# Kernel optimization log

Measured on AMD Instinct MI355X. Metric: run time of the kernel, lower is better.

The kernel has to match this reference:

```python
import jax, jax.numpy as jnp
import numpy as np

RADIUS = float(1.5 * 6 * 0.025 / 2.0)  # filter_extent / 2 = 0.1125
N_FLUID, N_BOX, K_F, K_B = 16000, 8000, 64, 32
KS = 4  # kernel size per axis -> 64 bins
EPS = 1e-12


def _radius_neighbors(q, p, radius, K, exclude_self=False):
    Nq = q.shape[0]
    idx = np.zeros((Nq, K), np.int32)
    mask = np.zeros((Nq, K), bool)
    r2 = radius * radius
    kth = min(K, p.shape[0] - 1)
    for s in range(0, Nq, 2048):
        e = min(s + 2048, Nq)
        d2 = ((q[s:e, None, :] - p[None, :, :]) ** 2).sum(-1)
        if exclude_self:
            d2[np.arange(e - s), np.arange(s, e)] = np.inf
        part = np.argpartition(d2, kth, axis=1)[:, :K].astype(np.int32)
        dk = np.take_along_axis(d2, part, 1)
        m = dk <= r2
        part[~m] = 0
        idx[s:e] = part
        mask[s:e] = m
    return idx, mask


def ball_to_cube(d):
    """Volume-preserving map unit ball -> unit cube [-1,1]^3 (Open3D ball_to_cube_volume_preserving)."""
    x, y, z = d[..., 0], d[..., 1], d[..., 2]
    sq = x * x + y * y + z * z
    norm = jnp.sqrt(sq)
    # --- sphere -> cylinder (radius 1, height 2) ---
    xy_sq = x * x + y * y
    polar = (1.25 * z * z) > xy_sq
    s_pol = jnp.sqrt(3.0 * norm / (norm + jnp.abs(z) + EPS))
    s_eq = norm / jnp.sqrt(xy_sq + EPS)
    s = jnp.where(polar, s_pol, s_eq)
    xc = x * s
    yc = y * s
    zc = jnp.where(polar, jnp.sign(z) * norm, 1.5 * z)
    zero = sq < EPS
    xc = jnp.where(zero, 0.0, xc)
    yc = jnp.where(zero, 0.0, yc)
    zc = jnp.where(zero, 0.0, zc)
    # --- cylinder -> cube: inverse Shirley-Chiu concentric map on the xy disc ---
    rxy = jnp.sqrt(xc * xc + yc * yc)
    xbig = jnp.abs(xc) >= jnp.abs(yc)
    safe_x = jnp.where(jnp.abs(xc) > EPS, xc, 1.0)
    safe_y = jnp.where(jnp.abs(yc) > EPS, yc, 1.0)
    four_over_pi = 4.0 / np.pi
    u1 = jnp.sign(xc) * rxy
    v1 = u1 * four_over_pi * jnp.arctan(yc / safe_x)
    v2 = jnp.sign(yc) * rxy
    u2 = v2 * four_over_pi * jnp.arctan(xc / safe_y)
    u = jnp.where(xbig, u1, u2)
    v = jnp.where(xbig, v1, v2)
    zero_xy = rxy < EPS
    u = jnp.where(zero_xy, 0.0, u)
    v = jnp.where(zero_xy, 0.0, v)
    return jnp.stack([u, v, zc], axis=-1)


def cconv(feat_src, pos_src, pos_q, nbr_idx, nbr_mask, filt, bias):
    """ContinuousConv: trilinear (align_corners=True) filter interpolation, poly6 window, no normalization."""
    N = pos_q.shape[0]
    kz, ky, kx, cin, cout = filt.shape
    pj = pos_src[nbr_idx]                       # [N,K,3]
    fj = feat_src[nbr_idx]                      # [N,K,Cin]
    d = (pj - pos_q[:, None, :]) / RADIUS       # normalized offsets in unit ball
    r_sqr = jnp.sum(d * d, axis=-1)             # [N,K]
    win = jnp.clip((1.0 - r_sqr) ** 3, 0.0, 1.0) * nbr_mask.astype(fj.dtype)
    u = ball_to_cube(d)                         # [N,K,3] in [-1,1]
    ks = jnp.asarray([kx, ky, kz], d.dtype)
    g = (u * 0.5 + 0.5) * (ks - 1.0)            # align_corners=True grid coords
    i0 = jnp.clip(jnp.floor(g), 0.0, ks - 2.0).astype(jnp.int32)  # [N,K,3]
    t = g - i0                                  # trilinear fractions
    Fflat = filt.reshape(kz * ky * kx, cin, cout)
    A = jnp.zeros((N, kz * ky * kx, cin), fj.dtype)   # per-query bin accumulator
    n_idx = jnp.arange(N)[:, None]
    for dz in (0, 1):
        for dy in (0, 1):
            for dx in (0, 1):
                w = ((t[..., 0] if dx else 1.0 - t[..., 0])
                     * (t[..., 1] if dy else 1.0 - t[..., 1])
                     * (t[..., 2] if dz else 1.0 - t[..., 2])) * win
                bins = ((i0[..., 2] + dz) * ky + (i0[..., 1] + dy)) * kx + (i0[..., 0] + dx)
                A = A.at[n_idx, bins].add(w[..., None] * fj)
    return jnp.einsum('nbc,bco->no', A, Fflat) + bias


def _forward(pos, vel, box, box_feats,
             w_conv0_fluid, b_conv0_fluid, w_conv0_obstacle, b_conv0_obstacle,
             w_dense0, b_dense0, w_conv1, b_conv1, w_dense1, b_dense1,
             w_conv2, b_conv2, w_dense2, b_dense2,
             nbr_fluid_idx, nbr_fluid_mask, nbr_box_idx, nbr_box_mask):
    fluid_feats = jnp.concatenate([jnp.ones_like(pos[:, :1]), vel], axis=-1)  # [N,4]
    a_cf = cconv(fluid_feats, pos, pos, nbr_fluid_idx, nbr_fluid_mask, w_conv0_fluid, b_conv0_fluid)
    a_df = fluid_feats @ w_dense0 + b_dense0
    a_co = cconv(box_feats, box, pos, nbr_box_idx, nbr_box_mask, w_conv0_obstacle, b_conv0_obstacle)
    feats = jnp.concatenate([a_co, a_cf, a_df], axis=-1)                      # [N,96]
    inp1 = jax.nn.relu(feats)
    ans1 = cconv(inp1, pos, pos, nbr_fluid_idx, nbr_fluid_mask, w_conv1, b_conv1) + inp1 @ w_dense1 + b_dense1
    inp2 = jax.nn.relu(ans1)
    ans2 = (cconv(inp2, pos, pos, nbr_fluid_idx, nbr_fluid_mask, w_conv2, b_conv2)
            + inp2 @ w_dense2 + b_dense2 + ans1)                               # residual (64==64)
    return ans2  # particle_feat = ans_convs[-2] returned by forward()


def setup_inputs() -> dict:
    rng = np.random.default_rng(0)
    L = 1.357  # cube side chosen so avg neighbor count within RADIUS is ~48
    pos = rng.uniform(0, L, (N_FLUID, 3)).astype(np.float32)
    box = rng.uniform(0, L, (N_BOX, 3)).astype(np.float32)
    vel = (0.5 * rng.standard_normal((N_FLUID, 3))).astype(np.float32)
    nrm = rng.standard_normal((N_BOX, 3)).astype(np.float32)
    box_feats = nrm / np.linalg.norm(nrm, axis=-1, keepdims=True)
    nf_idx, nf_mask = _radius_neighbors(pos, pos, RADIUS, K_F, exclude_self=True)
    nb_idx, nb_mask = _radius_neighbors(pos, box, RADIUS, K_B, exclude_self=False)

    def filt(cin, cout):
        s = (6.0 / (cin * KS ** 3 + cout)) ** 0.5
        return (s * rng.standard_normal((KS, KS, KS, cin, cout))).astype(np.float32)

    def lin(cin, cout):
        s = (6.0 / (cin + cout)) ** 0.5
        return (s * rng.standard_normal((cin, cout))).astype(np.float32)

    z = lambda c: np.zeros((c,), np.float32)
    inp = dict(
        pos=pos, vel=vel, box=box, box_feats=box_feats,
        w_conv0_fluid=filt(4, 32), b_conv0_fluid=z(32),
        w_conv0_obstacle=filt(3, 32), b_conv0_obstacle=z(32),
        w_dense0=lin(4, 32), b_dense0=z(32),
        w_conv1=filt(96, 64), b_conv1=z(64), w_dense1=lin(96, 64), b_dense1=z(64),
        w_conv2=filt(64, 64), b_conv2=z(64), w_dense2=lin(64, 64), b_dense2=z(64),
        nbr_fluid_idx=nf_idx, nbr_fluid_mask=nf_mask,
        nbr_box_idx=nb_idx, nbr_box_mask=nb_mask,
    )
    return {k: jnp.asarray(v) for k, v in inp.items()}


def reference(pos, vel, box, box_feats,
              w_conv0_fluid, b_conv0_fluid, w_conv0_obstacle, b_conv0_obstacle,
              w_dense0, b_dense0, w_conv1, b_conv1, w_dense1, b_dense1,
              w_conv2, b_conv2, w_dense2, b_dense2,
              nbr_fluid_idx, nbr_fluid_mask, nbr_box_idx, nbr_box_mask):
    return _forward(pos, vel, box, box_feats,
                    w_conv0_fluid, b_conv0_fluid, w_conv0_obstacle, b_conv0_obstacle,
                    w_dense0, b_dense0, w_conv1, b_conv1, w_dense1, b_dense1,
                    w_conv2, b_conv2, w_dense2, b_dense2,
                    nbr_fluid_idx, nbr_fluid_mask, nbr_box_idx, nbr_box_mask)
```

## Files before the change

kernel.cpp:

```cpp
#include <hip/hip_runtime.h>
#include <cstdint>

#define DEVFN __device__ __forceinline__

using hh8 = __attribute__((ext_vector_type(8))) _Float16;
using f4  = __attribute__((ext_vector_type(4))) float;

constexpr float RAD  = 0.1125f;
constexpr float R2C  = RAD * RAD;
constexpr float EPSF = 1e-12f;
constexpr float FOPI = 1.27323954473516268615f;

DEVFN float sgnf(float a){ return (a > 0.f) ? 1.f : ((a < 0.f) ? -1.f : 0.f); }

DEVFN unsigned short f2h(float f){
  _Float16 h = (_Float16)f;
  union { _Float16 h; unsigned short u; } x; x.h = h; return x.u;
}
DEVFN hh8 ld_hh8(const unsigned short* p){ return *(const hh8*)p; }

DEVFN void nbr_geom(float ddx, float ddy, float ddz, float factor, int* bins, float* w8)
{
  float x = ddx / RAD, y = ddy / RAD, z = ddz / RAD;
  float sq = x*x + y*y + z*z;
  float omr = 1.f - sq;
  float win = (omr > 0.f) ? omr*omr*omr : 0.f;
  win *= factor;
  float nrm   = sqrtf(sq);
  float xy_sq = x*x + y*y;
  bool  polar = (1.25f*z*z) > xy_sq;
  float s = polar ? sqrtf(3.f*nrm/(nrm + fabsf(z) + EPSF))
                  : (nrm / sqrtf(xy_sq + EPSF));
  float xc = x*s, yc = y*s;
  float zc = polar ? (sgnf(z)*nrm) : (1.5f*z);
  if (sq < EPSF){ xc = 0.f; yc = 0.f; zc = 0.f; }
  float rxy  = sqrtf(xc*xc + yc*yc);
  bool  xbig = fabsf(xc) >= fabsf(yc);
  float sx = (fabsf(xc) > EPSF) ? xc : 1.f;
  float sy = (fabsf(yc) > EPSF) ? yc : 1.f;
  float u1 = sgnf(xc)*rxy;
  float v1 = u1 * FOPI * atanf(yc / sx);
  float v2 = sgnf(yc)*rxy;
  float u2 = v2 * FOPI * atanf(xc / sy);
  float u = xbig ? u1 : u2;
  float v = xbig ? v1 : v2;
  if (rxy < EPSF){ u = 0.f; v = 0.f; }
  float gx = (u *0.5f + 0.5f)*3.f;
  float gy = (v *0.5f + 0.5f)*3.f;
  float gz = (zc*0.5f + 0.5f)*3.f;
  float fx = fminf(fmaxf(floorf(gx), 0.f), 2.f);
  float fy = fminf(fmaxf(floorf(gy), 0.f), 2.f);
  float fz = fminf(fmaxf(floorf(gz), 0.f), 2.f);
  int ix = (int)fx, iy = (int)fy, iz = (int)fz;
  float tx = gx - fx, ty = gy - fy, tz = gz - fz;
  float wx[2] = {1.f - tx, tx};
  float wy[2] = {1.f - ty, ty};
  float wz[2] = {1.f - tz, tz};
  #pragma unroll
  for (int dz2 = 0; dz2 < 2; ++dz2)
    #pragma unroll
    for (int dy2 = 0; dy2 < 2; ++dy2)
      #pragma unroll
      for (int dx2 = 0; dx2 < 2; ++dx2){
        int c = (dz2 << 2) | (dy2 << 1) | dx2;
        bins[c] = ((iz + dz2)*4 + (iy + dy2))*4 + (ix + dx2);
        w8[c]   = wx[dx2]*wy[dy2]*wz[dz2]*win;
      }
}

__global__ __launch_bounds__(256)
void k_conv0(const float* __restrict__ pos, const float* __restrict__ vel,
             const float* __restrict__ box, const float* __restrict__ boxf,
             const float* __restrict__ Wfilt, const float* __restrict__ bcf,
             const float* __restrict__ Ofilt, const float* __restrict__ bco,
             const float* __restrict__ Wd0, const float* __restrict__ bd0,
             const int* __restrict__ nfi, const int* __restrict__ nbi,
             int KB, float* __restrict__ inp1)
{
  const int n = blockIdx.x, t = threadIdx.x;
  const int lane = t & 63, w = t >> 6, r = lane & 15, h = lane >> 4;

  __shared__ __align__(16) unsigned short LWf[64*64];
  __shared__ __align__(16) unsigned short LWo[64*32];
  __shared__ __align__(16) unsigned short LBf[16*64];
  __shared__ __align__(16) unsigned short LBo[16*32];
  __shared__ float Af[64*4];
  __shared__ float Ao[64*3];
  __shared__ int gjf[64]; __shared__ int gjo[32];
  __shared__ float red[256];

  const float qx = pos[3*n], qy = pos[3*n+1], qz = pos[3*n+2];
  int bins[8]; float w8[8];

  if (w == 0){
    const int k = lane;
    const int j = nfi[(size_t)n*64 + k];
    const float ddx = pos[3*j] - qx, ddy = pos[3*j+1] - qy, ddz = pos[3*j+2] - qz;
    const float d2 = ddx*ddx + ddy*ddy + ddz*ddz;
    unsigned long long zm = __ballot(j == 0);
    int fz = __ffsll(zm) - 1;
    float factor = (j != 0) ? 1.f : ((k == fz && d2 <= R2C && n != 0) ? 1.f : 0.f);
    nbr_geom(ddx, ddy, ddz, factor, bins, w8);
    gjf[k] = j;
  } else if (w == 1){
    const int k = lane;
    const bool act = k < KB;
    const int j = act ? nbi[(size_t)n*KB + k] : 1;
    float ddx = 0.f, ddy = 0.f, ddz = 0.f, d2 = 1e30f;
    if (act){
      ddx = box[3*j] - qx; ddy = box[3*j+1] - qy; ddz = box[3*j+2] - qz;
      d2 = ddx*ddx + ddy*ddy + ddz*ddz;
    }
    unsigned long long zm = __ballot(act && j == 0);
    int fz = __ffsll(zm) - 1;
    float factor = (j != 0) ? 1.f : ((k == fz && d2 <= R2C) ? 1.f : 0.f);
    nbr_geom(ddx, ddy, ddz, factor, bins, w8);
    if (act) gjo[k] = j;
  } else {
    int4 z4 = make_int4(0,0,0,0);
    for (int i = t-128; i < 512; i += 128) *(int4*)&LWf[i*8] = z4;
    for (int i = t-128; i < 256; i += 128) *(int4*)&LWo[i*8] = z4;
    if (t-128 < 128) *(int4*)&LBf[(t-128)*8] = z4;
    if (t-128 <  64) *(int4*)&LBo[(t-128)*8] = z4;
  }
  __syncthreads();

  if (w == 0){
    #pragma unroll
    for (int q = 0; q < 8; ++q){
      int b = bins[q];
      LWf[b*64 + (lane ^ ((b&7)<<3))] = f2h(w8[q]);
    }
  } else if (w == 1){
    if (lane < KB){
      #pragma unroll
      for (int q = 0; q < 8; ++q){
        int b = bins[q];
        LWo[b*32 + (lane ^ ((b&3)<<3))] = f2h(w8[q]);
      }
    }
  } else if (w == 2){
    const int k = lane; const int j = gjf[k];
    LBf[0*64 + k] = f2h(1.f);
    LBf[1*64 + (k ^ 8)]  = f2h(vel[3*j]);
    LBf[2*64 + (k ^ 16)] = f2h(vel[3*j+1]);
    LBf[3*64 + (k ^ 24)] = f2h(vel[3*j+2]);
  } else {
    if (lane < KB){
      const int k = lane; const int j = gjo[k];
      LBo[0*32 + k]        = f2h(boxf[3*j]);
      LBo[1*32 + (k ^ 8)]  = f2h(boxf[3*j+1]);
      LBo[2*32 + (k ^ 16)] = f2h(boxf[3*j+2]);
    }
  }
  __syncthreads();

  f4 aF = {0.f,0.f,0.f,0.f}, aO = {0.f,0.f,0.f,0.f};
  {
    const int b = 16*w + r;
    #pragma unroll
    for (int ks = 0; ks < 2; ++ks){
      hh8 a  = ld_hh8(&LWf[b*64 + (((ks*4+h) ^ (b&7))<<3)]);
      hh8 bb = ld_hh8(&LBf[r*64 + (((ks*4+h) ^ (r&7))<<3)]);
      aF = __builtin_amdgcn_mfma_f32_16x16x32_f16(a, bb, aF, 0,0,0);
    }
    hh8 a2 = ld_hh8(&LWo[b*32 + ((h ^ (b&3))<<3)]);
    hh8 b2 = ld_hh8(&LBo[r*32 + ((h ^ (r&3))<<3)]);
    aO = __builtin_amdgcn_mfma_f32_16x16x32_f16(a2, b2, aO, 0,0,0);
  }
  #pragma unroll
  for (int rr = 0; rr < 4; ++rr){
    int b2 = 16*w + h*4 + rr;
    if (r < 4) Af[b2*4 + r] = aF[rr];
    if (r < 3) Ao[b2*3 + r] = aO[rr];
  }
  __syncthreads();

  const int o = t & 31, g = t >> 5;
  float p1 = 0.f;
  for (int b2 = g*8; b2 < g*8 + 8; ++b2)
    #pragma unroll
    for (int c = 0; c < 4; ++c)
      p1 += Af[b2*4 + c] * Wfilt[(b2*4 + c)*32 + o];
  red[t] = p1;
  __syncthreads();
  float a_cf = 0.f;
  if (t < 32){ for (int g2 = 0; g2 < 8; ++g2) a_cf += red[t + 32*g2]; }
  __syncthreads();
  float p2 = 0.f;
  for (int b2 = g*8; b2 < g*8 + 8; ++b2)
    #pragma unroll
    for (int c = 0; c < 3; ++c)
      p2 += Ao[b2*3 + c] * Ofilt[(b2*3 + c)*32 + o];
  red[t] = p2;
  __syncthreads();
  if (t < 32){
    float a_co = 0.f;
    for (int g2 = 0; g2 < 8; ++g2) a_co += red[t + 32*g2];
    const float vx = vel[3*n], vy = vel[3*n+1], vz = vel[3*n+2];
    const float a_df = Wd0[t] + Wd0[32 + t]*vx + Wd0[64 + t]*vy + Wd0[96 + t]*vz;
    const size_t base = (size_t)n * 96;
    inp1[base +      t] = fmaxf(a_co + bco[t], 0.f);
    inp1[base + 32 + t] = fmaxf(a_cf + bcf[t], 0.f);
    inp1[base + 64 + t] = fmaxf(a_df + bd0[t], 0.f);
  }
}

template<int C>
__global__ __launch_bounds__(256)
void k1_scatter(const float* __restrict__ pos, const float* __restrict__ feat,
                const int* __restrict__ nfi, int n0, unsigned short* __restrict__ Abuf)
{
  constexpr int Kpad = 64*C + C + (C == 96 ? 32 : 0);
  constexpr int CT = C/16;
  const int nloc = blockIdx.x;
  const int n = n0 + nloc;
  const int t = threadIdx.x;
  const int lane = t & 63, w = t >> 6, r = lane & 15, h = lane >> 4;

  __shared__ __align__(16) unsigned short sh[4096 + C*64];
  unsigned short* W  = sh;
  unsigned short* BT = sh + 4096;
  __shared__ int gj[64];

  int bins[8]; float w8[8];
  if (w == 0){
    const float qx = pos[3*n], qy = pos[3*n+1], qz = pos[3*n+2];
    const int k = lane;
    const int j = nfi[(size_t)n*64 + k];
    const float ddx = pos[3*j] - qx, ddy = pos[3*j+1] - qy, ddz = pos[3*j+2] - qz;
    const float d2 = ddx*ddx + ddy*ddy + ddz*ddz;
    unsigned long long zm = __ballot(j == 0);
    int fz = __ffsll(zm) - 1;
    float factor = (j != 0) ? 1.f : ((k == fz && d2 <= R2C && n != 0) ? 1.f : 0.f);
    nbr_geom(ddx, ddy, ddz, factor, bins, w8);
    gj[k] = j;
  } else {
    int4 z4 = make_int4(0,0,0,0);
    for (int i = t - 64; i < 512; i += 192) *(int4*)&W[i*8] = z4;
  }
  __syncthreads();

  if (w == 0){
    #pragma unroll
    for (int q = 0; q < 8; ++q){
      int b = bins[q];
      W[b*64 + (lane ^ ((b&7)<<3))] = f2h(w8[q]);
    }
  }
  for (int i = t; i < C*64; i += 256){
    int k = i / C, c = i - k*C;
    int j = gj[k];
    BT[c*64 + (k ^ ((c&7)<<3))] = f2h(feat[(size_t)j*C + c]);
  }
  __syncthreads();

  f4 acc[CT];
  #pragma unroll
  for (int ct = 0; ct < CT; ++ct) acc[ct] = f4{0.f,0.f,0.f,0.f};
  const int b = 16*w + r;
  #pragma unroll
  for (int ks = 0; ks < 2; ++ks){
    hh8 a = ld_hh8(&W[b*64 + (((ks*4+h) ^ (b&7))<<3)]);
    #pragma unroll
    for (int ct = 0; ct < CT; ++ct){
      int c = ct*16 + r;
      hh8 bb = ld_hh8(&BT[c*64 + (((ks*4+h) ^ (c&7))<<3)]);
      acc[ct] = __builtin_amdgcn_mfma_f32_16x16x32_f16(a, bb, acc[ct], 0,0,0);
    }
  }
  __syncthreads();

  unsigned short* Aout = sh;
  #pragma unroll
  for (int ct = 0; ct < CT; ++ct){
    int c = ct*16 + r;
    #pragma unroll
    for (int rr = 0; rr < 4; ++rr){
      int b2 = 16*w + h*4 + rr;
      Aout[b2*C + c] = f2h(acc[ct][rr]);
    }
  }
  if (t < C) Aout[64*C + t] = f2h(feat[(size_t)n*C + t]);
  if constexpr (C == 96){
    if (t >= 96 && t < 128) Aout[6240 + t - 96] = 0;
  }
  __syncthreads();

  const int key = nloc & 7;
  const size_t rowBase = (size_t)nloc * Kpad;
  for (int ch = t; ch < Kpad/8; ch += 256){
    int4 v = *(const int4*)&Aout[ch*8];
    *(int4*)&Abuf[rowBase + (size_t)(ch ^ key)*8] = v;
  }
}

__global__ __launch_bounds__(256)
void k_bpack(const float* __restrict__ F, const float* __restrict__ Wd,
             int kSplit, int Cd, int Kpad, unsigned short* __restrict__ BpkT)
{
  int idx = blockIdx.x*256 + threadIdx.x;
  int chunks = Kpad/8;
  if (idx >= 64*chunks) return;
  int o = idx / chunks, ch = idx - o*chunks;
  union { int4 v; unsigned short u[8]; } pk;
  #pragma unroll
  for (int e = 0; e < 8; ++e){
    int kp = ch*8 + e;
    float f = 0.f;
    if (kp < kSplit)            f = F[(size_t)kp*64 + o];
    else if (kp < kSplit + Cd)  f = Wd[(size_t)(kp - kSplit)*64 + o];
    pk.u[e] = f2h(f);
  }
  *(int4*)&BpkT[((size_t)o*chunks + (ch ^ (o&7)))*8] = pk.v;
}

__global__ __launch_bounds__(256)
void k2_gemm(const unsigned short* __restrict__ Abuf, const unsigned short* __restrict__ BpkT,
             float* __restrict__ partial, int n0, int CHa, int Kpad, int ktot,
             int sB, int NF)
{
  const int t = threadIdx.x;
  const int lane = t & 63, w = t >> 6, r = lane & 15, h = lane >> 4;
  const int seg = blockIdx.y;
  const int ks0 = seg*sB;
  const int ks1 = (ks0 + sB < ktot) ? (ks0 + sB) : ktot;
  const int rowBase = blockIdx.x * 128;

  __shared__ __align__(16) unsigned short Asub[128*64];
  __shared__ __align__(16) unsigned short Bsub[64*64];

  f4 acc[2][4];
  #pragma unroll
  for (int i = 0; i < 2; ++i)
    #pragma unroll
    for (int j = 0; j < 4; ++j) acc[i][j] = f4{0.f,0.f,0.f,0.f};

  for (int ks = ks0; ks < ks1; ++ks){
    #pragma unroll
    for (int i = 0; i < 4; ++i){
      int lin = i*256 + t;
      int row = lin >> 3, lc = lin & 7;
      int grow = rowBase + row; if (grow >= CHa) grow = CHa - 1;
      int4 v = *(const int4*)&Abuf[(size_t)grow*Kpad + ks*64 + lc*8];
      *(int4*)&Asub[lin*8] = v;
    }
    #pragma unroll
    for (int i = 0; i < 2; ++i){
      int lin = i*256 + t;
      int o = lin >> 3, lc = lin & 7;
      int4 v = *(const int4*)&BpkT[(size_t)o*Kpad + ks*64 + lc*8];
      *(int4*)&Bsub[lin*8] = v;
    }
    __syncthreads();
    #pragma unroll
    for (int kh = 0; kh < 2; ++kh){
      hh8 a0 = ld_hh8(&Asub[(w*32 +      r)*64 + (((kh*4+h) ^ (r&7))<<3)]);
      hh8 a1 = ld_hh8(&Asub[(w*32 + 16 + r)*64 + (((kh*4+h) ^ (r&7))<<3)]);
      #pragma unroll
      for (int nt = 0; nt < 4; ++nt){
        hh8 bb = ld_hh8(&Bsub[(nt*16 + r)*64 + (((kh*4+h) ^ (r&7))<<3)]);
        acc[0][nt] = __builtin_amdgcn_mfma_f32_16x16x32_f16(a0, bb, acc[0][nt], 0,0,0);
        acc[1][nt] = __builtin_amdgcn_mfma_f32_16x16x32_f16(a1, bb, acc[1][nt], 0,0,0);
      }
    }
    __syncthreads();
  }

  #pragma unroll
  for (int mt = 0; mt < 2; ++mt)
    #pragma unroll
    for (int rr = 0; rr < 4; ++rr){
      int m = rowBase + w*32 + mt*16 + h*4 + rr;
      if (m < CHa){
        float* op = partial + ((size_t)seg*NF + n0 + m)*64;
        #pragma unroll
        for (int nt = 0; nt < 4; ++nt)
          op[nt*16 + r] = acc[mt][nt][rr];
      }
    }
}

__global__ __launch_bounds__(256)
void k_epi(const float* __restrict__ partial, const float* __restrict__ bc,
           const float* __restrict__ bd, const float* __restrict__ resid,
           float* __restrict__ outRaw, float* __restrict__ outRelu, int total)
{
  const int i = blockIdx.x*256 + threadIdx.x;
  if (i >= total) return;
  float v = 0.f;
  #pragma unroll
  for (int s = 0; s < 8; ++s) v += partial[(size_t)s*total + i];
  const int o = i & 63;
  v += bc[o] + bd[o];
  if (resid)   v += resid[i];
  if (outRaw)  outRaw[i]  = v;
  if (outRelu) outRelu[i] = fmaxf(v, 0.f);
}

extern "C" void kernel_launch(void* const* d_in, const int* in_sizes, int n_in,
                              void* d_out, int out_size, void* d_ws, size_t ws_size,
                              hipStream_t stream)
{
  const float* pos  = (const float*)d_in[0];
  const float* vel  = (const float*)d_in[1];
  const float* box  = (const float*)d_in[2];
  const float* boxf = (const float*)d_in[3];
  const float* Wc0f = (const float*)d_in[4];
  const float* bc0f = (const float*)d_in[5];
  const float* Wc0o = (const float*)d_in[6];
  const float* bc0o = (const float*)d_in[7];
  const float* Wd0  = (const float*)d_in[8];
  const float* bd0  = (const float*)d_in[9];
  const float* Wc1  = (const float*)d_in[10];
  const float* bc1  = (const float*)d_in[11];
  const float* Wd1  = (const float*)d_in[12];
  const float* bd1  = (const float*)d_in[13];
  const float* Wc2  = (const float*)d_in[14];
  const float* bc2  = (const float*)d_in[15];
  const float* Wd2  = (const float*)d_in[16];
  const float* bd2  = (const float*)d_in[17];
  const int* nfi = (const int*)d_in[18];
  const int* nbi = (const int*)d_in[20];
  const int NF = in_sizes[0]/3;
  const int KB = in_sizes[20]/NF;
  float* out = (float*)d_out;

  char* wsb = (char*)d_ws;
  auto alloc = [&](size_t bytes){ char* p = wsb; wsb += (bytes + 255) & ~(size_t)255; return p; };
  float* inp1    = (float*)alloc((size_t)NF*96*4);
  float* ans1    = (float*)alloc((size_t)NF*64*4);
  float* inp2    = (float*)alloc((size_t)NF*64*4);
  float* partial = (float*)alloc((size_t)8*NF*64*4);
  unsigned short* Bpk1 = (unsigned short*)alloc((size_t)64*6272*2);
  unsigned short* Bpk2 = (unsigned short*)alloc((size_t)64*4160*2);
  unsigned short* Abuf = (unsigned short*)wsb;
  size_t usedB = (size_t)(wsb - (char*)d_ws);
  size_t availUS = (ws_size > usedB) ? (ws_size - usedB)/2 : 0;

  auto chunkOf = [&](int Kpad)->int{
    long long c = (long long)(availUS / (size_t)Kpad);
    if (c >= NF) return NF;
    int ch = (int)c & ~127;
    if (ch < 128) ch = 128;
    return ch;
  };

  k_conv0<<<NF, 256, 0, stream>>>(pos, vel, box, boxf, Wc0f, bc0f, Wc0o, bc0o,
                                  Wd0, bd0, nfi, nbi, KB, inp1);
  k_bpack<<<(64*784 + 255)/256, 256, 0, stream>>>(Wc1, Wd1, 6144, 96, 6272, Bpk1);
  k_bpack<<<(64*520 + 255)/256, 256, 0, stream>>>(Wc2, Wd2, 4096, 64, 4160, Bpk2);

  {
    int CH = chunkOf(6272);
    for (int n0 = 0; n0 < NF; n0 += CH){
      int CHa = (n0 + CH < NF) ? CH : (NF - n0);
      k1_scatter<96><<<CHa, 256, 0, stream>>>(pos, inp1, nfi, n0, Abuf);
      int tiles = (CHa + 127)/128;
      k2_gemm<<<dim3(tiles, 8), 256, 0, stream>>>(Abuf, Bpk1, partial, n0, CHa,
                                                  6272, 98, 13, NF);
    }
    k_epi<<<(NF*64 + 255)/256, 256, 0, stream>>>(partial, bc1, bd1, nullptr,
                                                 ans1, inp2, NF*64);
  }
  {
    int CH = chunkOf(4160);
    for (int n0 = 0; n0 < NF; n0 += CH){
      int CHa = (n0 + CH < NF) ? CH : (NF - n0);
      k1_scatter<64><<<CHa, 256, 0, stream>>>(pos, inp2, nfi, n0, Abuf);
      int tiles = (CHa + 127)/128;
      k2_gemm<<<dim3(tiles, 8), 256, 0, stream>>>(Abuf, Bpk2, partial, n0, CHa,
                                                  4160, 65, 9, NF);
    }
    k_epi<<<(NF*64 + 255)/256, 256, 0, stream>>>(partial, bc2, bd2, ans1,
                                                 out, nullptr, NF*64);
  }
}
```

Before: 265.6 us.

## Store intermediate activations as fp16 and overlap feature gather with geometry

Intermediate feature buffers inp1 and inp2 are now written as fp16 by the producer kernels instead of fp32. The scatter kernel reads them directly without converting. The gather is restructured so warps 1-3 each take one neighbor row per lane and fill the transposed tile, while warp 0 does the neighbor geometry in parallel. This halves the bytes moved in the random neighbor gathers and removes the per-element conversions and divisions, at the cost of rounding the stored activations to fp16 earlier.

Result: slower. 330.4 us (+24.4%).

```diff
diff --git a/kernel.cpp b/kernel.cpp
--- a/kernel.cpp
+++ b/kernel.cpp
@@ -16,6 +16,9 @@
 DEVFN unsigned short f2h(float f){
   _Float16 h = (_Float16)f;
   union { _Float16 h; unsigned short u; } x; x.h = h; return x.u;
+}
+DEVFN float h2f(unsigned short u){
+  union { _Float16 h; unsigned short u; } x; x.u = u; return (float)x.h;
 }
 DEVFN hh8 ld_hh8(const unsigned short* p){ return *(const hh8*)p; }
 
@@ -75,7 +78,7 @@
              const float* __restrict__ Ofilt, const float* __restrict__ bco,
              const float* __restrict__ Wd0, const float* __restrict__ bd0,
              const int* __restrict__ nfi, const int* __restrict__ nbi,
-             int KB, float* __restrict__ inp1)
+             int KB, unsigned short* __restrict__ inp1)
 {
   const int n = blockIdx.x, t = threadIdx.x;
   const int lane = t & 63, w = t >> 6, r = lane & 15, h = lane >> 4;
@@ -200,15 +203,15 @@
     const float vx = vel[3*n], vy = vel[3*n+1], vz = vel[3*n+2];
     const float a_df = Wd0[t] + Wd0[32 + t]*vx + Wd0[64 + t]*vy + Wd0[96 + t]*vz;
     const size_t base = (size_t)n * 96;
-    inp1[base +      t] = fmaxf(a_co + bco[t], 0.f);
-    inp1[base + 32 + t] = fmaxf(a_cf + bcf[t], 0.f);
-    inp1[base + 64 + t] = fmaxf(a_df + bd0[t], 0.f);
+    inp1[base +      t] = f2h(fmaxf(a_co + bco[t], 0.f));
+    inp1[base + 32 + t] = f2h(fmaxf(a_cf + bcf[t], 0.f));
+    inp1[base + 64 + t] = f2h(fmaxf(a_df + bd0[t], 0.f));
   }
 }
 
 template<int C>
 __global__ __launch_bounds__(256)
-void k1_scatter(const float* __restrict__ pos, const float* __restrict__ feat,
+void k1_scatter(const float* __restrict__ pos, const unsigned short* __restrict__ feat,
                 const int* __restrict__ nfi, int n0, unsigned short* __restrict__ Abuf)
 {
   constexpr int Kpad = 64*C + C + (C == 96 ? 32 : 0);
@@ -223,18 +226,12 @@
   unsigned short* BT = sh + 4096;
   __shared__ int gj[64];
 
-  int bins[8]; float w8[8];
+  int jreg = 0; float qx=0.f,qy=0.f,qz=0.f,px=0.f,py=0.f,pz=0.f;
   if (w == 0){
-    const float qx = pos[3*n], qy = pos[3*n+1], qz = pos[3*n+2];
-    const int k = lane;
-    const int j = nfi[(size_t)n*64 + k];
-    const float ddx = pos[3*j] - qx, ddy = pos[3*j+1] - qy, ddz = pos[3*j+2] - qz;
-    const float d2 = ddx*ddx + ddy*ddy + ddz*ddz;
-    unsigned long long zm = __ballot(j == 0);
-    int fz = __ffsll(zm) - 1;
-    float factor = (j != 0) ? 1.f : ((k == fz && d2 <= R2C && n != 0) ? 1.f : 0.f);
-    nbr_geom(ddx, ddy, ddz, factor, bins, w8);
-    gj[k] = j;
+    jreg = nfi[(size_t)n*64 + lane];
+    gj[lane] = jreg;
+    qx = pos[3*n]; qy = pos[3*n+1]; qz = pos[3*n+2];
+    px = pos[3*jreg]; py = pos[3*jreg+1]; pz = pos[3*jreg+2];
   } else {
     int4 z4 = make_int4(0,0,0,0);
     for (int i = t - 64; i < 512; i += 192) *(int4*)&W[i*8] = z4;
@@ -242,16 +239,26 @@
   __syncthreads();
 
   if (w == 0){
+    const int k = lane;
+    const float ddx = px - qx, ddy = py - qy, ddz = pz - qz;
+    const float d2 = ddx*ddx + ddy*ddy + ddz*ddz;
+    unsigned long long zm = __ballot(jreg == 0);
+    int fz = __ffsll(zm) - 1;
+    float factor = (jreg != 0) ? 1.f : ((k == fz && d2 <= R2C && n != 0) ? 1.f : 0.f);
+    int bins[8]; float w8[8];
+    nbr_geom(ddx, ddy, ddz, factor, bins, w8);
     #pragma unroll
     for (int q = 0; q < 8; ++q){
       int b = bins[q];
       W[b*64 + (lane ^ ((b&7)<<3))] = f2h(w8[q]);
     }
-  }
-  for (int i = t; i < C*64; i += 256){
-    int k = i / C, c = i - k*C;
-    int j = gj[k];
-    BT[c*64 + (k ^ ((c&7)<<3))] = f2h(feat[(size_t)j*C + c]);
+  } else {
+    const int k = lane;
+    const unsigned short* fr = feat + (size_t)gj[k]*C;
+    #pragma unroll 4
+    for (int c = w - 1; c < C; c += 3){
+      BT[(c<<6) + (k ^ ((c&7)<<3))] = fr[c];
+    }
   }
   __syncthreads();
 
@@ -281,7 +288,7 @@
       Aout[b2*C + c] = f2h(acc[ct][rr]);
     }
   }
-  if (t < C) Aout[64*C + t] = f2h(feat[(size_t)n*C + t]);
+  if (t < C) Aout[64*C + t] = feat[(size_t)n*C + t];
   if constexpr (C == 96){
     if (t >= 96 && t < 128) Aout[6240 + t - 96] = 0;
   }
@@ -384,7 +391,7 @@
 __global__ __launch_bounds__(256)
 void k_epi(const float* __restrict__ partial, const float* __restrict__ bc,
            const float* __restrict__ bd, const float* __restrict__ resid,
-           float* __restrict__ outRaw, float* __restrict__ outRelu, int total)
+           float* __restrict__ outRaw, unsigned short* __restrict__ outRelu, int total)
 {
   const int i = blockIdx.x*256 + threadIdx.x;
   if (i >= total) return;
@@ -395,7 +402,7 @@
   v += bc[o] + bd[o];
   if (resid)   v += resid[i];
   if (outRaw)  outRaw[i]  = v;
-  if (outRelu) outRelu[i] = fmaxf(v, 0.f);
+  if (outRelu) outRelu[i] = f2h(fmaxf(v, 0.f));
 }
 
 extern "C" void kernel_launch(void* const* d_in, const int* in_sizes, int n_in,
@@ -428,9 +435,9 @@
 
   char* wsb = (char*)d_ws;
   auto alloc = [&](size_t bytes){ char* p = wsb; wsb += (bytes + 255) & ~(size_t)255; return p; };
-  float* inp1    = (float*)alloc((size_t)NF*96*4);
+  unsigned short* inp1 = (unsigned short*)alloc((size_t)NF*96*2);
   float* ans1    = (float*)alloc((size_t)NF*64*4);
-  float* inp2    = (float*)alloc((size_t)NF*64*4);
+  unsigned short* inp2 = (unsigned short*)alloc((size_t)NF*64*2);
   float* partial = (float*)alloc((size_t)8*NF*64*4);
   unsigned short* Bpk1 = (unsigned short*)alloc((size_t)64*6272*2);
   unsigned short* Bpk2 = (unsigned short*)alloc((size_t)64*4160*2);
```
